# Kernel tuning notes

Hardware: AMD Instinct MI355X
Metric: run time of the kernel (lower is better)

The kernel has to match this reference:

```python
import jax, jax.numpy as jnp
import numpy as np

G = 8            # n_group
C = 256          # input_dim / channels
N_MEM = C // G   # 32
ALPHA = 0.4      # w_alpha
EPS = 1e-5
SLOPE = 0.01     # LeakyReLU negative slope


def _lrelu(x):
    return jnp.where(x >= 0, x, SLOPE * x)


def _mlp(x, ws, bs):
    # torch nn.Linear convention: y = x @ W.T + b; lrelu on all but last layer
    n = len(ws)
    for i in range(n):
        x = x @ ws[i].T + bs[i]
        if i < n - 1:
            x = _lrelu(x)
    return x


def _wct(c_A, s_B, mask, ct_ws, ct_bs, mu_ws, mu_bs):
    B, Cc, H, W = c_A.shape
    n_mem = Cc // G
    # style -> per-group coloring matrices  (Get.coloring, vectorized over groups)
    s_CT = _mlp(s_B.reshape(B * G, n_mem), ct_ws, ct_bs).reshape(B, G, n_mem, n_mem)
    D = jnp.sqrt(jnp.sum(s_CT ** 2, axis=2, keepdims=True))        # [B,G,1,n_mem]
    U = s_CT / D                                                    # column-normalized
    UDU = jnp.einsum('bgij,bgkj->bgik', s_CT, U)                    # [B,G,n_mem,n_mem]
    # torch.cat(U_arr, dim=0) is group-major: index g*B+b
    eigen_s = jnp.transpose(U, (1, 0, 2, 3)).reshape(G * B, n_mem, n_mem)
    X = jnp.tile(UDU.reshape(B, Cc, n_mem), (1, 1, G)) * mask       # [B,C,C]
    s_mu = _mlp(s_B, mu_ws, mu_bs)[:, :, None, None]                # [B,C,1,1]
    # per-group covariance of mean-centered content
    c_g = jnp.transpose(c_A, (1, 0, 2, 3)).reshape(G, n_mem, B * H * W)
    c_g = c_g - jnp.mean(c_g, axis=2, keepdims=True)
    cov_c = jnp.einsum('gin,gjn->gij', c_g, c_g) / (B * H * W - 1) \
        + EPS * jnp.eye(n_mem, dtype=c_A.dtype)
    # centered content, reinterpreted as [B, C, H*W] (matches torch view/permute)
    whitend = jnp.transpose(c_g.reshape(Cc, B, H * W), (1, 0, 2))
    colored = jnp.einsum('bcd,bdn->bcn', X, whitend).reshape(B, Cc, H, W)
    out = ALPHA * (colored + s_mu) + (1.0 - ALPHA) * c_A
    return out, cov_c, eigen_s


def setup_inputs():
    key = jax.random.key(0)
    ks = jax.random.split(key, 16)
    B, H, W = 4, 128, 128
    c_A = jax.random.normal(ks[0], (B, C, H, W), dtype=jnp.float32)
    s_B = jax.random.normal(ks[1], (B, C), dtype=jnp.float32)
    # block-diagonal group mask [1, C, C]
    m = np.zeros((C, C), dtype=np.float32)
    for g in range(G):
        m[g * N_MEM:(g + 1) * N_MEM, g * N_MEM:(g + 1) * N_MEM] = 1.0
    mask = jnp.asarray(m)[None]

    def lin(k, o, i):
        return jax.random.normal(k, (o, i), dtype=jnp.float32) * (1.0 / np.sqrt(i))

    inp = {'c_A': c_A, 's_B': s_B, 'mask': mask}
    dims_ct = [(256, 32), (256, 256), (256, 256), (256, 256), (1024, 256)]
    for j, (o, i) in enumerate(dims_ct):
        inp['ct_w%d' % j] = lin(ks[2 + j], o, i)
        inp['ct_b%d' % j] = jnp.zeros((o,), dtype=jnp.float32)
    dims_mu = [(256, 256), (256, 256), (256, 256)]
    for j, (o, i) in enumerate(dims_mu):
        inp['mu_w%d' % j] = lin(ks[8 + j], o, i)
        inp['mu_b%d' % j] = jnp.zeros((o,), dtype=jnp.float32)
    return inp


def reference(c_A, s_B, mask, ct_w0, ct_b0, ct_w1, ct_b1, ct_w2, ct_b2,
              ct_w3, ct_b3, ct_w4, ct_b4, mu_w0, mu_b0, mu_w1, mu_b1,
              mu_w2, mu_b2):
    ct_ws = (ct_w0, ct_w1, ct_w2, ct_w3, ct_w4)
    ct_bs = (ct_b0, ct_b1, ct_b2, ct_b3, ct_b4)
    mu_ws = (mu_w0, mu_w1, mu_w2)
    mu_bs = (mu_b0, mu_b1, mu_b2)
    return _wct(c_A, s_B, mask, ct_ws, ct_bs, mu_ws, mu_bs)
```

## Files before the change

### kernel.cpp

```cpp
#include <hip/hip_runtime.h>
#include <hip/hip_bf16.h>

typedef __bf16 bf16x8 __attribute__((ext_vector_type(8)));
typedef float  f32x16 __attribute__((ext_vector_type(16)));

#define ALPHA_W 0.4f
#define NTOT 65536.0f

#define OUT_MAIN 16777216
#define OUT_COV  (OUT_MAIN)
#define OUT_EIG  (OUT_MAIN + 8192)

#define WS_PSXY  0
#define WS_PSX   524288
#define WS_XA    540672
#define WS_XB    548864
#define WS_MUA   557056
#define WS_MUB   558080
#define WS_SMU   559104
#define WS_CT    560128

struct WP {
    const float* cw0; const float* cb0;
    const float* cw1; const float* cb1;
    const float* cw2; const float* cb2;
    const float* cw3; const float* cb3;
    const float* cw4; const float* cb4;
    const float* mw0; const float* mb0;
    const float* mw1; const float* mb1;
    const float* mw2; const float* mb2;
};

struct SJ { const float* X; const float* W; const float* B; float* Y; int ld; int act; };

__device__ __forceinline__ float lrelu(float x) { return x >= 0.f ? x : 0.01f * x; }

template<int ROWS, int IN, int KS, int NCB, int ACT>
__device__ __forceinline__ void lin_block(const float* __restrict__ X,
                                          const float* __restrict__ Wg,
                                          const float* __restrict__ Bs,
                                          float* __restrict__ Y, int ld,
                                          int bidl, int tid) {
    constexpr int SL = IN / KS;
    constexpr int SF4 = SL / 4;
    int s = tid % KS;
    int r = (tid / KS) % ROWS;
    int c = tid / (KS * ROWS);
    int col = bidl * NCB + c;
    const float4* wp = (const float4*)(Wg + (size_t)col * IN + s * SL);
    const float4* xp = (const float4*)(X + r * IN + s * SL);
    float a0 = 0.f, a1 = 0.f, a2 = 0.f, a3 = 0.f;
    #pragma unroll
    for (int i = 0; i < SF4; ++i) {
        float4 wv = wp[i];
        float4 xv = xp[i];
        a0 = fmaf(wv.x, xv.x, a0); a1 = fmaf(wv.y, xv.y, a1);
        a2 = fmaf(wv.z, xv.z, a2); a3 = fmaf(wv.w, xv.w, a3);
    }
    float v = (a0 + a1) + (a2 + a3);
    #pragma unroll
    for (int m = 1; m < KS; m <<= 1) v += __shfl_xor(v, m, 64);
    if (s == 0) {
        float o = v + Bs[col];
        if (ACT) o = lrelu(o);
        Y[(size_t)r * ld + col] = o;
    }
}

__global__ __launch_bounds__(256, 2) void front(const float* __restrict__ cA,
                                                const float* __restrict__ sB,
                                                WP wp,
                                                float* __restrict__ pSXY,
                                                float* __restrict__ pSX,
                                                float* __restrict__ XA,
                                                float* __restrict__ MUA) {
    int bid = blockIdx.x;
    int tid = threadIdx.x;
    if (bid < 64) {
        if (bid < 32) {
            lin_block<32, 32, 1, 8, 1>(sB, wp.cw0, wp.cb0, XA, 256, bid, tid);
        } else {
            lin_block<4, 256, 8, 8, 1>(sB, wp.mw0, wp.mb0, MUA, 256, bid - 32, tid);
        }
        return;
    }
    int gbid = bid - 64;
    int g = gbid >> 6, slice = gbid & 63;
    int w = tid >> 6, l = tid & 63;
    int col = l & 31, kq = l >> 5;
    int nbase = slice * 1024 + w * 256;
    int b = nbase >> 14, hw0 = nbase & 16383;
    const float* base = cA + (((size_t)(b * 256 + g * 32 + col)) << 14) + hw0 + kq * 8;
    f32x16 acc;
    #pragma unroll
    for (int r = 0; r < 16; r++) acc[r] = 0.f;
    float s0 = 0.f, s1 = 0.f;
    #pragma unroll 8
    for (int it = 0; it < 16; ++it) {
        float4 f0 = *(const float4*)(base + it * 16);
        float4 f1 = *(const float4*)(base + it * 16 + 4);
        s0 += (f0.x + f0.y) + (f0.z + f0.w);
        s1 += (f1.x + f1.y) + (f1.z + f1.w);
        bf16x8 v;
        v[0] = (__bf16)f0.x; v[1] = (__bf16)f0.y; v[2] = (__bf16)f0.z; v[3] = (__bf16)f0.w;
        v[4] = (__bf16)f1.x; v[5] = (__bf16)f1.y; v[6] = (__bf16)f1.z; v[7] = (__bf16)f1.w;
        acc = __builtin_amdgcn_mfma_f32_32x32x16_bf16(v, v, acc, 0, 0, 0);
    }
    __shared__ float red[4][1024];
    __shared__ float sxr[4][64];
    sxr[w][l] = s0 + s1;
    #pragma unroll
    for (int r = 0; r < 16; r++) {
        int i = (r & 3) + 8 * (r >> 2) + 4 * kq;
        red[w][i * 32 + col] = acc[r];
    }
    __syncthreads();
    for (int e = tid; e < 1024; e += 256)
        pSXY[(size_t)gbid * 1024 + e] = red[0][e] + red[1][e] + red[2][e] + red[3][e];
    if (tid < 32) {
        float v = 0.f;
        #pragma unroll
        for (int ww = 0; ww < 4; ww++) v += sxr[ww][tid] + sxr[ww][tid + 32];
        pSX[gbid * 32 + tid] = v;
    }
}

__global__ __launch_bounds__(256) void stage(SJ a, SJ m, int nbA) {
    int bid = blockIdx.x, tid = threadIdx.x;
    if (bid < nbA) {
        if (a.act) lin_block<32, 256, 4, 2, 1>(a.X, a.W, a.B, a.Y, a.ld, bid, tid);
        else       lin_block<32, 256, 4, 2, 0>(a.X, a.W, a.B, a.Y, a.ld, bid, tid);
    } else {
        int bl = bid - nbA;
        if (m.act) lin_block<4, 256, 8, 8, 1>(m.X, m.W, m.B, m.Y, m.ld, bl, tid);
        else       lin_block<4, 256, 8, 8, 0>(m.X, m.W, m.B, m.Y, m.ld, bl, tid);
    }
}

__global__ __launch_bounds__(256) void color_fused(const float* __restrict__ cA,
                                                   const float* __restrict__ CT,
                                                   const float* __restrict__ SMU,
                                                   const float* __restrict__ pSX,
                                                   const float* __restrict__ pSXY,
                                                   float* __restrict__ out) {
    __shared__ float sct[32 * 33];
    __shared__ float sctd[32 * 33];
    __shared__ float Ml[1024];
    __shared__ float tl[32];
    __shared__ float sxg[32];
    __shared__ float dinv[32];
    __shared__ float xs[2][2048];
    int bid = blockIdx.x;
    int tid = threadIdx.x;

    if (bid >= 1024) {
        int g = bid - 1024;
        if (tid < 32) {
            float s = 0.f;
            #pragma unroll
            for (int sl = 0; sl < 64; sl++) s += pSX[(g * 64 + sl) * 32 + tid];
            sxg[tid] = s * (1.0f / NTOT);
        }
        __syncthreads();
        float* cov = out + OUT_COV + (size_t)g * 1024;
        for (int e = tid; e < 1024; e += 256) {
            float s = 0.f;
            #pragma unroll
            for (int sl = 0; sl < 64; sl++) s += pSXY[(size_t)(g * 64 + sl) * 1024 + e];
            int i = e >> 5, jj = e & 31;
            float vv = (s - NTOT * sxg[i] * sxg[jj]) * (1.0f / (NTOT - 1.0f));
            if (i == jj) vv += 1e-5f;
            cov[e] = vv;
        }
        return;
    }

    int bg = bid >> 5, chunk = bid & 31;
    int b = bg >> 3, g = bg & 7;

    for (int e = tid; e < 1024; e += 256) sct[(e >> 5) * 33 + (e & 31)] = CT[(size_t)bg * 1024 + e];
    if (tid < 32) {
        float s = 0.f;
        #pragma unroll
        for (int sl = 0; sl < 64; sl++) s += pSX[(g * 64 + sl) * 32 + tid];
        sxg[tid] = s * (1.0f / NTOT);
    }
    __syncthreads();
    if (tid < 32) {
        float s = 0.f;
        #pragma unroll
        for (int i = 0; i < 32; i++) { float v = sct[i * 33 + tid]; s = fmaf(v, v, s); }
        dinv[tid] = 1.0f / sqrtf(s);
    }
    __syncthreads();
    for (int e = tid; e < 1024; e += 256) {
        int i = e >> 5, j = e & 31;
        sctd[i * 33 + j] = sct[i * 33 + j] * dinv[j];
    }
    __syncthreads();
    if (chunk == 0) {
        float* eig = out + OUT_EIG + (size_t)(g * 4 + b) * 1024;
        for (int e = tid; e < 1024; e += 256) eig[e] = sctd[(e >> 5) * 33 + (e & 31)];
    }
    for (int e = tid; e < 1024; e += 256) {
        int i = e >> 5, k = e & 31;
        float s = 0.f;
        #pragma unroll
        for (int j = 0; j < 32; j++) s = fmaf(sct[i * 33 + j], sctd[k * 33 + j], s);
        Ml[e] = ALPHA_W * s + (i == k ? (1.0f - ALPHA_W) : 0.0f);
    }
    __syncthreads();
    if (tid < 32) {
        float s = 0.f;
        #pragma unroll
        for (int k = 0; k < 32; k++) s = fmaf(Ml[tid * 32 + k], sxg[k], s);
        tl[tid] = ALPHA_W * SMU[bg * 32 + tid] - s + (1.0f - ALPHA_W) * sxg[tid];
    }

    int n = tid & 63, ih = tid >> 6;
    size_t cbase = (((size_t)(b * 256 + g * 32)) << 14) + chunk * 512;
    int srow = tid >> 3, scol = (tid & 7) * 8;
    size_t obase = (((size_t)(b * 256 + g * 32 + ih * 8)) << 14) + chunk * 512 + n;
    const float* src0 = cA + cbase + (size_t)srow * 16384 + scol;
    float4 u0 = *(const float4*)src0;
    float4 u1 = *(const float4*)(src0 + 4);
    for (int tile = 0; tile < 8; ++tile) {
        float* xd = &xs[tile & 1][srow * 64 + scol];
        *(float4*)xd = u0;
        *(float4*)(xd + 4) = u1;
        if (tile < 7) {
            const float* src = cA + cbase + (size_t)srow * 16384 + (tile + 1) * 64 + scol;
            u0 = *(const float4*)src;
            u1 = *(const float4*)(src + 4);
        }
        __syncthreads();
        const float* xb = xs[tile & 1];
        float acc[8];
        #pragma unroll
        for (int i = 0; i < 8; i++) acc[i] = tl[ih * 8 + i];
        #pragma unroll
        for (int k = 0; k < 32; k++) {
            float xv = xb[k * 64 + n];
            #pragma unroll
            for (int i = 0; i < 8; i++) acc[i] = fmaf(Ml[(ih * 8 + i) * 32 + k], xv, acc[i]);
        }
        float* dst = out + obase + tile * 64;
        #pragma unroll
        for (int i = 0; i < 8; i++) dst[(size_t)i << 14] = acc[i];
    }
}

extern "C" void kernel_launch(void* const* d_in, const int* in_sizes, int n_in,
                              void* d_out, int out_size, void* d_ws, size_t ws_size,
                              hipStream_t stream) {
    (void)in_sizes; (void)n_in; (void)out_size; (void)ws_size;
    const float* cA = (const float*)d_in[0];
    const float* sB = (const float*)d_in[1];
    WP wp;
    wp.cw0 = (const float*)d_in[3];  wp.cb0 = (const float*)d_in[4];
    wp.cw1 = (const float*)d_in[5];  wp.cb1 = (const float*)d_in[6];
    wp.cw2 = (const float*)d_in[7];  wp.cb2 = (const float*)d_in[8];
    wp.cw3 = (const float*)d_in[9];  wp.cb3 = (const float*)d_in[10];
    wp.cw4 = (const float*)d_in[11]; wp.cb4 = (const float*)d_in[12];
    wp.mw0 = (const float*)d_in[13]; wp.mb0 = (const float*)d_in[14];
    wp.mw1 = (const float*)d_in[15]; wp.mb1 = (const float*)d_in[16];
    wp.mw2 = (const float*)d_in[17]; wp.mb2 = (const float*)d_in[18];
    float* W = (float*)d_ws;
    float* out = (float*)d_out;

    front<<<576, 256, 0, stream>>>(cA, sB, wp, W + WS_PSXY, W + WS_PSX,
                                   W + WS_XA, W + WS_MUA);
    SJ a, m;
    a = {W + WS_XA, wp.cw1, wp.cb1, W + WS_XB, 256, 1};
    m = {W + WS_MUA, wp.mw1, wp.mb1, W + WS_MUB, 256, 1};
    stage<<<160, 256, 0, stream>>>(a, m, 128);
    a = {W + WS_XB, wp.cw2, wp.cb2, W + WS_XA, 256, 1};
    m = {W + WS_MUB, wp.mw2, wp.mb2, W + WS_SMU, 256, 0};
    stage<<<160, 256, 0, stream>>>(a, m, 128);
    a = {W + WS_XA, wp.cw3, wp.cb3, W + WS_XB, 256, 1};
    stage<<<128, 256, 0, stream>>>(a, a, 128);
    a = {W + WS_XB, wp.cw4, wp.cb4, W + WS_CT, 1024, 0};
    stage<<<512, 256, 0, stream>>>(a, a, 512);

    color_fused<<<1032, 256, 0, stream>>>(cA, W + WS_CT, W + WS_SMU,
                                          W + WS_PSX, W + WS_PSXY, out);
}
```

Measured before the change: 197.3 us.

## Fuse MLP stages into front kernel with grid barriers and precompute coloring matrix

New measurement: 253.9 us. 28.7% more time.

```diff
diff --git a/kernel.cpp b/kernel.cpp
--- a/kernel.cpp
+++ b/kernel.cpp
@@ -19,6 +19,8 @@
 #define WS_MUB   558080
 #define WS_SMU   559104
 #define WS_CT    560128
+#define WS_M     592896
+#define WS_BAR   625664
 
 struct WP {
     const float* cw0; const float* cb0;
@@ -31,9 +33,19 @@
     const float* mw2; const float* mb2;
 };
 
-struct SJ { const float* X; const float* W; const float* B; float* Y; int ld; int act; };
-
 __device__ __forceinline__ float lrelu(float x) { return x >= 0.f ? x : 0.01f * x; }
+
+__device__ __forceinline__ void mlp_bar(int* bar, int phase, int nb, int tid) {
+    __syncthreads();
+    if (tid == 0) {
+        __threadfence();
+        __hip_atomic_fetch_add(&bar[phase], 1, __ATOMIC_RELEASE, __HIP_MEMORY_SCOPE_AGENT);
+        while (__hip_atomic_load(&bar[phase], __ATOMIC_ACQUIRE, __HIP_MEMORY_SCOPE_AGENT) < nb)
+            __builtin_amdgcn_s_sleep(2);
+        __threadfence();
+    }
+    __syncthreads();
+}
 
 template<int ROWS, int IN, int KS, int NCB, int ACT>
 __device__ __forceinline__ void lin_block(const float* __restrict__ X,
@@ -67,89 +79,132 @@
     }
 }
 
+__global__ void zero_bar(int* bar) {
+    if (threadIdx.x < 16) bar[threadIdx.x] = 0;
+}
+
 __global__ __launch_bounds__(256, 2) void front(const float* __restrict__ cA,
                                                 const float* __restrict__ sB,
                                                 WP wp,
-                                                float* __restrict__ pSXY,
-                                                float* __restrict__ pSX,
-                                                float* __restrict__ XA,
-                                                float* __restrict__ MUA) {
+                                                float* __restrict__ Wf,
+                                                float* __restrict__ out) {
+    __shared__ float smem[4352];
     int bid = blockIdx.x;
     int tid = threadIdx.x;
+
     if (bid < 64) {
+        float* XA  = Wf + WS_XA;
+        float* XB  = Wf + WS_XB;
+        float* MUA = Wf + WS_MUA;
+        float* MUB = Wf + WS_MUB;
+        float* SMU = Wf + WS_SMU;
+        float* CT  = Wf + WS_CT;
+        int* bar = (int*)(Wf + WS_BAR);
+        if (bid < 32) lin_block<32, 32, 1, 8, 1>(sB, wp.cw0, wp.cb0, XA, 256, bid, tid);
+        else          lin_block<4, 256, 8, 8, 1>(sB, wp.mw0, wp.mb0, MUA, 256, bid - 32, tid);
+        mlp_bar(bar, 0, 64, tid);
+        lin_block<32, 256, 2, 4, 1>(XA, wp.cw1, wp.cb1, XB, 256, bid, tid);
+        lin_block<4, 256, 16, 4, 1>(MUA, wp.mw1, wp.mb1, MUB, 256, bid, tid);
+        mlp_bar(bar, 1, 64, tid);
+        lin_block<32, 256, 2, 4, 1>(XB, wp.cw2, wp.cb2, XA, 256, bid, tid);
+        lin_block<4, 256, 16, 4, 0>(MUB, wp.mw2, wp.mb2, SMU, 256, bid, tid);
+        mlp_bar(bar, 2, 64, tid);
+        lin_block<32, 256, 2, 4, 1>(XA, wp.cw3, wp.cb3, XB, 256, bid, tid);
+        mlp_bar(bar, 3, 64, tid);
+        lin_block<32, 256, 2, 4, 0>(XB, wp.cw4,          wp.cb4,       CT,       1024, bid, tid);
+        lin_block<32, 256, 2, 4, 0>(XB, wp.cw4 + 65536,  wp.cb4 + 256, CT + 256, 1024, bid, tid);
+        lin_block<32, 256, 2, 4, 0>(XB, wp.cw4 + 131072, wp.cb4 + 512, CT + 512, 1024, bid, tid);
+        lin_block<32, 256, 2, 4, 0>(XB, wp.cw4 + 196608, wp.cb4 + 768, CT + 768, 1024, bid, tid);
+        mlp_bar(bar, 4, 64, tid);
         if (bid < 32) {
-            lin_block<32, 32, 1, 8, 1>(sB, wp.cw0, wp.cb0, XA, 256, bid, tid);
-        } else {
-            lin_block<4, 256, 8, 8, 1>(sB, wp.mw0, wp.mb0, MUA, 256, bid - 32, tid);
-        }
-        return;
-    }
-    int gbid = bid - 64;
-    int g = gbid >> 6, slice = gbid & 63;
-    int w = tid >> 6, l = tid & 63;
-    int col = l & 31, kq = l >> 5;
-    int nbase = slice * 1024 + w * 256;
-    int b = nbase >> 14, hw0 = nbase & 16383;
-    const float* base = cA + (((size_t)(b * 256 + g * 32 + col)) << 14) + hw0 + kq * 8;
-    f32x16 acc;
-    #pragma unroll
-    for (int r = 0; r < 16; r++) acc[r] = 0.f;
-    float s0 = 0.f, s1 = 0.f;
-    #pragma unroll 8
-    for (int it = 0; it < 16; ++it) {
-        float4 f0 = *(const float4*)(base + it * 16);
-        float4 f1 = *(const float4*)(base + it * 16 + 4);
-        s0 += (f0.x + f0.y) + (f0.z + f0.w);
-        s1 += (f1.x + f1.y) + (f1.z + f1.w);
-        bf16x8 v;
-        v[0] = (__bf16)f0.x; v[1] = (__bf16)f0.y; v[2] = (__bf16)f0.z; v[3] = (__bf16)f0.w;
-        v[4] = (__bf16)f1.x; v[5] = (__bf16)f1.y; v[6] = (__bf16)f1.z; v[7] = (__bf16)f1.w;
-        acc = __builtin_amdgcn_mfma_f32_32x32x16_bf16(v, v, acc, 0, 0, 0);
-    }
-    __shared__ float red[4][1024];
-    __shared__ float sxr[4][64];
-    sxr[w][l] = s0 + s1;
-    #pragma unroll
-    for (int r = 0; r < 16; r++) {
-        int i = (r & 3) + 8 * (r >> 2) + 4 * kq;
-        red[w][i * 32 + col] = acc[r];
-    }
-    __syncthreads();
-    for (int e = tid; e < 1024; e += 256)
-        pSXY[(size_t)gbid * 1024 + e] = red[0][e] + red[1][e] + red[2][e] + red[3][e];
-    if (tid < 32) {
-        float v = 0.f;
-        #pragma unroll
-        for (int ww = 0; ww < 4; ww++) v += sxr[ww][tid] + sxr[ww][tid + 32];
-        pSX[gbid * 32 + tid] = v;
-    }
-}
-
-__global__ __launch_bounds__(256) void stage(SJ a, SJ m, int nbA) {
-    int bid = blockIdx.x, tid = threadIdx.x;
-    if (bid < nbA) {
-        if (a.act) lin_block<32, 256, 4, 2, 1>(a.X, a.W, a.B, a.Y, a.ld, bid, tid);
-        else       lin_block<32, 256, 4, 2, 0>(a.X, a.W, a.B, a.Y, a.ld, bid, tid);
-    } else {
-        int bl = bid - nbA;
-        if (m.act) lin_block<4, 256, 8, 8, 1>(m.X, m.W, m.B, m.Y, m.ld, bl, tid);
-        else       lin_block<4, 256, 8, 8, 0>(m.X, m.W, m.B, m.Y, m.ld, bl, tid);
+            float* sct  = smem;
+            float* uu   = smem + 1056;
+            float* dinv = smem + 2112;
+            int b = bid >> 3, g = bid & 7;
+            for (int e = tid; e < 1024; e += 256)
+                sct[(e >> 5) * 33 + (e & 31)] = CT[(size_t)bid * 1024 + e];
+            __syncthreads();
+            if (tid < 32) {
+                float s = 0.f;
+                #pragma unroll
+                for (int i = 0; i < 32; i++) { float v = sct[i * 33 + tid]; s = fmaf(v, v, s); }
+                dinv[tid] = 1.0f / sqrtf(s);
+            }
+            __syncthreads();
+            float* eig = out + OUT_EIG + (size_t)(g * 4 + b) * 1024;
+            for (int e = tid; e < 1024; e += 256) {
+                int i = e >> 5, j = e & 31;
+                float u = sct[i * 33 + j] * dinv[j];
+                uu[i * 33 + j] = u;
+                eig[e] = u;
+            }
+            __syncthreads();
+            float* Mo = Wf + WS_M + (size_t)bid * 1024;
+            for (int e = tid; e < 1024; e += 256) {
+                int i = e >> 5, k = e & 31;
+                float s = 0.f;
+                #pragma unroll
+                for (int j = 0; j < 32; j++) s = fmaf(sct[i * 33 + j], uu[k * 33 + j], s);
+                Mo[e] = ALPHA_W * s + (i == k ? (1.0f - ALPHA_W) : 0.0f);
+            }
+            __syncthreads();
+        }
+    }
+
+    float* pSXY = Wf + WS_PSXY;
+    float* pSX  = Wf + WS_PSX;
+    int gbid = bid;
+    {
+        int g = gbid >> 6, slice = gbid & 63;
+        int w = tid >> 6, l = tid & 63;
+        int col = l & 31, kq = l >> 5;
+        int nbase = slice * 1024 + w * 256;
+        int b = nbase >> 14, hw0 = nbase & 16383;
+        const float* base = cA + (((size_t)(b * 256 + g * 32 + col)) << 14) + hw0 + kq * 8;
+        f32x16 acc;
+        #pragma unroll
+        for (int r = 0; r < 16; r++) acc[r] = 0.f;
+        float s0 = 0.f, s1 = 0.f;
+        #pragma unroll 8
+        for (int it = 0; it < 16; ++it) {
+            float4 f0 = *(const float4*)(base + it * 16);
+            float4 f1 = *(const float4*)(base + it * 16 + 4);
+            s0 += (f0.x + f0.y) + (f0.z + f0.w);
+            s1 += (f1.x + f1.y) + (f1.z + f1.w);
+            bf16x8 v;
+            v[0] = (__bf16)f0.x; v[1] = (__bf16)f0.y; v[2] = (__bf16)f0.z; v[3] = (__bf16)f0.w;
+            v[4] = (__bf16)f1.x; v[5] = (__bf16)f1.y; v[6] = (__bf16)f1.z; v[7] = (__bf16)f1.w;
+            acc = __builtin_amdgcn_mfma_f32_32x32x16_bf16(v, v, acc, 0, 0, 0);
+        }
+        float* red = smem;
+        float* sxr = smem + 4096;
+        sxr[w * 64 + l] = s0 + s1;
+        #pragma unroll
+        for (int r = 0; r < 16; r++) {
+            int i = (r & 3) + 8 * (r >> 2) + 4 * kq;
+            red[w * 1024 + i * 32 + col] = acc[r];
+        }
+        __syncthreads();
+        for (int e = tid; e < 1024; e += 256)
+            pSXY[(size_t)gbid * 1024 + e] = red[e] + red[1024 + e] + red[2048 + e] + red[3072 + e];
+        if (tid < 32) {
+            float v = 0.f;
+            #pragma unroll
+            for (int ww = 0; ww < 4; ww++) v += sxr[ww * 64 + tid] + sxr[ww * 64 + tid + 32];
+            pSX[gbid * 32 + tid] = v;
+        }
     }
 }
 
 __global__ __launch_bounds__(256) void color_fused(const float* __restrict__ cA,
-                                                   const float* __restrict__ CT,
+                                                   const float* __restrict__ M,
                                                    const float* __restrict__ SMU,
                                                    const float* __restrict__ pSX,
                                                    const float* __restrict__ pSXY,
                                                    float* __restrict__ out) {
-    __shared__ float sct[32 * 33];
-    __shared__ float sctd[32 * 33];
     __shared__ float Ml[1024];
     __shared__ float tl[32];
     __shared__ float sxg[32];
-    __shared__ float dinv[32];
-    __shared__ float xs[2][2048];
     int bid = blockIdx.x;
     int tid = threadIdx.x;
 
@@ -178,7 +233,7 @@
     int bg = bid >> 5, chunk = bid & 31;
     int b = bg >> 3, g = bg & 7;
 
-    for (int e = tid; e < 1024; e += 256) sct[(e >> 5) * 33 + (e & 31)] = CT[(size_t)bg * 1024 + e];
+    for (int e = tid; e < 1024; e += 256) Ml[e] = M[(size_t)bg * 1024 + e];
     if (tid < 32) {
         float s = 0.f;
         #pragma unroll
@@ -189,64 +244,52 @@
     if (tid < 32) {
         float s = 0.f;
         #pragma unroll
-        for (int i = 0; i < 32; i++) { float v = sct[i * 33 + tid]; s = fmaf(v, v, s); }
-        dinv[tid] = 1.0f / sqrtf(s);
-    }
-    __syncthreads();
-    for (int e = tid; e < 1024; e += 256) {
-        int i = e >> 5, j = e & 31;
-        sctd[i * 33 + j] = sct[i * 33 + j] * dinv[j];
-    }
-    __syncthreads();
-    if (chunk == 0) {
-        float* eig = out + OUT_EIG + (size_t)(g * 4 + b) * 1024;
-        for (int e = tid; e < 1024; e += 256) eig[e] = sctd[(e >> 5) * 33 + (e & 31)];
-    }
-    for (int e = tid; e < 1024; e += 256) {
-        int i = e >> 5, k = e & 31;
-        float s = 0.f;
-        #pragma unroll
-        for (int j = 0; j < 32; j++) s = fmaf(sct[i * 33 + j], sctd[k * 33 + j], s);
-        Ml[e] = ALPHA_W * s + (i == k ? (1.0f - ALPHA_W) : 0.0f);
-    }
-    __syncthreads();
-    if (tid < 32) {
-        float s = 0.f;
-        #pragma unroll
         for (int k = 0; k < 32; k++) s = fmaf(Ml[tid * 32 + k], sxg[k], s);
         tl[tid] = ALPHA_W * SMU[bg * 32 + tid] - s + (1.0f - ALPHA_W) * sxg[tid];
     }
-
-    int n = tid & 63, ih = tid >> 6;
-    size_t cbase = (((size_t)(b * 256 + g * 32)) << 14) + chunk * 512;
-    int srow = tid >> 3, scol = (tid & 7) * 8;
-    size_t obase = (((size_t)(b * 256 + g * 32 + ih * 8)) << 14) + chunk * 512 + n;
-    const float* src0 = cA + cbase + (size_t)srow * 16384 + scol;
-    float4 u0 = *(const float4*)src0;
-    float4 u1 = *(const float4*)(src0 + 4);
-    for (int tile = 0; tile < 8; ++tile) {
-        float* xd = &xs[tile & 1][srow * 64 + scol];
-        *(float4*)xd = u0;
-        *(float4*)(xd + 4) = u1;
-        if (tile < 7) {
-            const float* src = cA + cbase + (size_t)srow * 16384 + (tile + 1) * 64 + scol;
-            u0 = *(const float4*)src;
-            u1 = *(const float4*)(src + 4);
-        }
-        __syncthreads();
-        const float* xb = xs[tile & 1];
-        float acc[8];
-        #pragma unroll
-        for (int i = 0; i < 8; i++) acc[i] = tl[ih * 8 + i];
-        #pragma unroll
-        for (int k = 0; k < 32; k++) {
-            float xv = xb[k * 64 + n];
-            #pragma unroll
-            for (int i = 0; i < 8; i++) acc[i] = fmaf(Ml[(ih * 8 + i) * 32 + k], xv, acc[i]);
-        }
-        float* dst = out + obase + tile * 64;
-        #pragma unroll
-        for (int i = 0; i < 8; i++) dst[(size_t)i << 14] = acc[i];
+    __syncthreads();
+
+    int ci = tid >> 6;
+    int pj = tid & 63;
+    size_t rowbase = ((size_t)(b * 256 + g * 32)) << 14;
+    int px = chunk * 512 + pj * 8;
+    const float* xsrc = cA + rowbase + px;
+    float* dst = out + rowbase + (((size_t)ci * 8) << 14) + px;
+
+    float acc[8][8];
+    #pragma unroll
+    for (int c = 0; c < 8; ++c) {
+        float t0 = tl[ci * 8 + c];
+        #pragma unroll
+        for (int j = 0; j < 8; ++j) acc[c][j] = t0;
+    }
+    #pragma unroll 4
+    for (int k = 0; k < 32; ++k) {
+        const float* xk = xsrc + ((size_t)k << 14);
+        float4 x0 = *(const float4*)xk;
+        float4 x1 = *(const float4*)(xk + 4);
+        float xv0 = x0.x, xv1 = x0.y, xv2 = x0.z, xv3 = x0.w;
+        float xv4 = x1.x, xv5 = x1.y, xv6 = x1.z, xv7 = x1.w;
+        #pragma unroll
+        for (int c = 0; c < 8; ++c) {
+            float m = Ml[(ci * 8 + c) * 32 + k];
+            acc[c][0] = fmaf(m, xv0, acc[c][0]);
+            acc[c][1] = fmaf(m, xv1, acc[c][1]);
+            acc[c][2] = fmaf(m, xv2, acc[c][2]);
+            acc[c][3] = fmaf(m, xv3, acc[c][3]);
+            acc[c][4] = fmaf(m, xv4, acc[c][4]);
+            acc[c][5] = fmaf(m, xv5, acc[c][5]);
+            acc[c][6] = fmaf(m, xv6, acc[c][6]);
+            acc[c][7] = fmaf(m, xv7, acc[c][7]);
+        }
+    }
+    #pragma unroll
+    for (int c = 0; c < 8; ++c) {
+        float4 o0 = {acc[c][0], acc[c][1], acc[c][2], acc[c][3]};
+        float4 o1 = {acc[c][4], acc[c][5], acc[c][6], acc[c][7]};
+        float* d = dst + (((size_t)c) << 14);
+        *(float4*)d = o0;
+        *(float4*)(d + 4) = o1;
     }
 }
 
@@ -268,20 +311,8 @@
     float* W = (float*)d_ws;
     float* out = (float*)d_out;
 
-    front<<<576, 256, 0, stream>>>(cA, sB, wp, W + WS_PSXY, W + WS_PSX,
-                                   W + WS_XA, W + WS_MUA);
-    SJ a, m;
-    a = {W + WS_XA, wp.cw1, wp.cb1, W + WS_XB, 256, 1};
-    m = {W + WS_MUA, wp.mw1, wp.mb1, W + WS_MUB, 256, 1};
-    stage<<<160, 256, 0, stream>>>(a, m, 128);
-    a = {W + WS_XB, wp.cw2, wp.cb2, W + WS_XA, 256, 1};
-    m = {W + WS_MUB, wp.mw2, wp.mb2, W + WS_SMU, 256, 0};
-    stage<<<160, 256, 0, stream>>>(a, m, 128);
-    a = {W + WS_XA, wp.cw3, wp.cb3, W + WS_XB, 256, 1};
-    stage<<<128, 256, 0, stream>>>(a, a, 128);
-    a = {W + WS_XB, wp.cw4, wp.cb4, W + WS_CT, 1024, 0};
-    stage<<<512, 256, 0, stream>>>(a, a, 512);
-
-    color_fused<<<1032, 256, 0, stream>>>(cA, W + WS_CT, W + WS_SMU,
+    zero_bar<<<1, 64, 0, stream>>>((int*)(W + WS_BAR));
+    front<<<512, 256, 0, stream>>>(cA, sB, wp, W, out);
+    color_fused<<<1032, 256, 0, stream>>>(cA, W + WS_M, W + WS_SMU,
                                           W + WS_PSX, W + WS_PSXY, out);
 }
```

## Split coloring into finalize and register-tiled color kernel; parametrize covariance slicing

Applied to the files above, without the earlier changes.

Result: slower. 232.4 us (+17.8%).

```diff
diff --git a/kernel.cpp b/kernel.cpp
--- a/kernel.cpp
+++ b/kernel.cpp
@@ -10,15 +10,6 @@
 #define OUT_MAIN 16777216
 #define OUT_COV  (OUT_MAIN)
 #define OUT_EIG  (OUT_MAIN + 8192)
-
-#define WS_PSXY  0
-#define WS_PSX   524288
-#define WS_XA    540672
-#define WS_XB    548864
-#define WS_MUA   557056
-#define WS_MUB   558080
-#define WS_SMU   559104
-#define WS_CT    560128
 
 struct WP {
     const float* cw0; const float* cb0;
@@ -67,6 +58,7 @@
     }
 }
 
+template<int SPG>
 __global__ __launch_bounds__(256, 2) void front(const float* __restrict__ cA,
                                                 const float* __restrict__ sB,
                                                 WP wp,
@@ -84,11 +76,13 @@
         }
         return;
     }
+    constexpr int PSZ = 65536 / SPG;
+    constexpr int ITS = PSZ / 64;
     int gbid = bid - 64;
-    int g = gbid >> 6, slice = gbid & 63;
+    int g = gbid / SPG, slice = gbid % SPG;
     int w = tid >> 6, l = tid & 63;
     int col = l & 31, kq = l >> 5;
-    int nbase = slice * 1024 + w * 256;
+    int nbase = slice * PSZ + w * (PSZ / 4);
     int b = nbase >> 14, hw0 = nbase & 16383;
     const float* base = cA + (((size_t)(b * 256 + g * 32 + col)) << 14) + hw0 + kq * 8;
     f32x16 acc;
@@ -96,7 +90,7 @@
     for (int r = 0; r < 16; r++) acc[r] = 0.f;
     float s0 = 0.f, s1 = 0.f;
     #pragma unroll 8
-    for (int it = 0; it < 16; ++it) {
+    for (int it = 0; it < ITS; ++it) {
         float4 f0 = *(const float4*)(base + it * 16);
         float4 f1 = *(const float4*)(base + it * 16 + 4);
         s0 += (f0.x + f0.y) + (f0.z + f0.w);
@@ -137,123 +131,141 @@
     }
 }
 
-__global__ __launch_bounds__(256) void color_fused(const float* __restrict__ cA,
-                                                   const float* __restrict__ CT,
+template<int SPG>
+__global__ __launch_bounds__(256, 2) void finalize(const float* __restrict__ CT,
                                                    const float* __restrict__ SMU,
+                                                   const float* __restrict__ pSXY,
                                                    const float* __restrict__ pSX,
-                                                   const float* __restrict__ pSXY,
+                                                   float* __restrict__ M,
+                                                   float* __restrict__ T,
                                                    float* __restrict__ out) {
-    __shared__ float sct[32 * 33];
-    __shared__ float sctd[32 * 33];
-    __shared__ float Ml[1024];
-    __shared__ float tl[32];
+    int bid = blockIdx.x, t = threadIdx.x;
     __shared__ float sxg[32];
-    __shared__ float dinv[32];
-    __shared__ float xs[2][2048];
-    int bid = blockIdx.x;
-    int tid = threadIdx.x;
-
-    if (bid >= 1024) {
-        int g = bid - 1024;
-        if (tid < 32) {
+    if (bid < 32) {
+        int b = bid >> 3, g = bid & 7;
+        __shared__ float sct[32 * 33], uu[32 * 33], ud[32 * 33], dinv[32];
+        for (int e = t; e < 1024; e += 256) sct[(e >> 5) * 33 + (e & 31)] = CT[bid * 1024 + e];
+        if (t < 32) {
+            float s = 0.f;
+            #pragma unroll 8
+            for (int sl = 0; sl < SPG; sl++) s += pSX[(g * SPG + sl) * 32 + t];
+            sxg[t] = s * (1.0f / NTOT);
+        }
+        __syncthreads();
+        if (t < 32) {
             float s = 0.f;
             #pragma unroll
-            for (int sl = 0; sl < 64; sl++) s += pSX[(g * 64 + sl) * 32 + tid];
-            sxg[tid] = s * (1.0f / NTOT);
+            for (int i = 0; i < 32; i++) { float v = sct[i * 33 + t]; s = fmaf(v, v, s); }
+            dinv[t] = 1.0f / sqrtf(s);
+        }
+        __syncthreads();
+        float* eig = out + OUT_EIG + (size_t)(g * 4 + b) * 1024;
+        for (int e = t; e < 1024; e += 256) {
+            int i = e >> 5, jj = e & 31;
+            float u = sct[i * 33 + jj] * dinv[jj];
+            uu[i * 33 + jj] = u;
+            eig[e] = u;
+        }
+        __syncthreads();
+        float* Mo = M + (size_t)bid * 1024;
+        for (int e = t; e < 1024; e += 256) {
+            int i = e >> 5, k = e & 31;
+            float s = 0.f;
+            #pragma unroll
+            for (int jv = 0; jv < 32; jv++) s = fmaf(sct[i * 33 + jv], uu[k * 33 + jv], s);
+            ud[i * 33 + k] = s;
+            Mo[e] = ALPHA_W * s + (i == k ? (1.0f - ALPHA_W) : 0.0f);
+        }
+        __syncthreads();
+        if (t < 32) {
+            float s = 0.f;
+            #pragma unroll
+            for (int k = 0; k < 32; k++) s = fmaf(ud[t * 33 + k], sxg[k], s);
+            T[bid * 32 + t] = ALPHA_W * (SMU[bid * 32 + t] - s);
+        }
+    } else {
+        int g = bid - 32;
+        if (t < 32) {
+            float s = 0.f;
+            #pragma unroll 8
+            for (int sl = 0; sl < SPG; sl++) s += pSX[(g * SPG + sl) * 32 + t];
+            sxg[t] = s * (1.0f / NTOT);
         }
         __syncthreads();
         float* cov = out + OUT_COV + (size_t)g * 1024;
-        for (int e = tid; e < 1024; e += 256) {
-            float s = 0.f;
-            #pragma unroll
-            for (int sl = 0; sl < 64; sl++) s += pSXY[(size_t)(g * 64 + sl) * 1024 + e];
+        for (int e = t; e < 1024; e += 256) {
+            float s = 0.f;
+            #pragma unroll 8
+            for (int sl = 0; sl < SPG; sl++) s += pSXY[(size_t)(g * SPG + sl) * 1024 + e];
             int i = e >> 5, jj = e & 31;
             float vv = (s - NTOT * sxg[i] * sxg[jj]) * (1.0f / (NTOT - 1.0f));
             if (i == jj) vv += 1e-5f;
             cov[e] = vv;
         }
-        return;
-    }
-
+    }
+}
+
+__global__ __launch_bounds__(256) void color_k(const float* __restrict__ cA,
+                                               const float* __restrict__ M,
+                                               const float* __restrict__ T,
+                                               float* __restrict__ out) {
+    __shared__ float Ml[1024];
+    __shared__ float tl[32];
+    int bid = blockIdx.x;
+    int tid = threadIdx.x;
     int bg = bid >> 5, chunk = bid & 31;
     int b = bg >> 3, g = bg & 7;
 
-    for (int e = tid; e < 1024; e += 256) sct[(e >> 5) * 33 + (e & 31)] = CT[(size_t)bg * 1024 + e];
-    if (tid < 32) {
-        float s = 0.f;
+    for (int e = tid; e < 1024; e += 256) Ml[e] = M[(size_t)bg * 1024 + e];
+    if (tid < 32) tl[tid] = T[bg * 32 + tid];
+    __syncthreads();
+
+    int ci = tid >> 6;
+    int pj = tid & 63;
+    size_t rowbase = ((size_t)(b * 256 + g * 32)) << 14;
+    int px = chunk * 512 + pj * 8;
+    const float* xsrc = cA + rowbase + px;
+    float* dst = out + rowbase + (((size_t)ci * 8) << 14) + px;
+
+    float acc[8][8];
+    #pragma unroll
+    for (int c = 0; c < 8; ++c) {
+        float t0 = tl[ci * 8 + c];
         #pragma unroll
-        for (int sl = 0; sl < 64; sl++) s += pSX[(g * 64 + sl) * 32 + tid];
-        sxg[tid] = s * (1.0f / NTOT);
-    }
-    __syncthreads();
-    if (tid < 32) {
-        float s = 0.f;
+        for (int j = 0; j < 8; ++j) acc[c][j] = t0;
+    }
+    #pragma unroll 4
+    for (int k = 0; k < 32; ++k) {
+        const float* xk = xsrc + ((size_t)k << 14);
+        float4 x0 = *(const float4*)xk;
+        float4 x1 = *(const float4*)(xk + 4);
         #pragma unroll
-        for (int i = 0; i < 32; i++) { float v = sct[i * 33 + tid]; s = fmaf(v, v, s); }
-        dinv[tid] = 1.0f / sqrtf(s);
-    }
-    __syncthreads();
-    for (int e = tid; e < 1024; e += 256) {
-        int i = e >> 5, j = e & 31;
-        sctd[i * 33 + j] = sct[i * 33 + j] * dinv[j];
-    }
-    __syncthreads();
-    if (chunk == 0) {
-        float* eig = out + OUT_EIG + (size_t)(g * 4 + b) * 1024;
-        for (int e = tid; e < 1024; e += 256) eig[e] = sctd[(e >> 5) * 33 + (e & 31)];
-    }
-    for (int e = tid; e < 1024; e += 256) {
-        int i = e >> 5, k = e & 31;
-        float s = 0.f;
-        #pragma unroll
-        for (int j = 0; j < 32; j++) s = fmaf(sct[i * 33 + j], sctd[k * 33 + j], s);
-        Ml[e] = ALPHA_W * s + (i == k ? (1.0f - ALPHA_W) : 0.0f);
-    }
-    __syncthreads();
-    if (tid < 32) {
-        float s = 0.f;
-        #pragma unroll
-        for (int k = 0; k < 32; k++) s = fmaf(Ml[tid * 32 + k], sxg[k], s);
-        tl[tid] = ALPHA_W * SMU[bg * 32 + tid] - s + (1.0f - ALPHA_W) * sxg[tid];
-    }
-
-    int n = tid & 63, ih = tid >> 6;
-    size_t cbase = (((size_t)(b * 256 + g * 32)) << 14) + chunk * 512;
-    int srow = tid >> 3, scol = (tid & 7) * 8;
-    size_t obase = (((size_t)(b * 256 + g * 32 + ih * 8)) << 14) + chunk * 512 + n;
-    const float* src0 = cA + cbase + (size_t)srow * 16384 + scol;
-    float4 u0 = *(const float4*)src0;
-    float4 u1 = *(const float4*)(src0 + 4);
-    for (int tile = 0; tile < 8; ++tile) {
-        float* xd = &xs[tile & 1][srow * 64 + scol];
-        *(float4*)xd = u0;
-        *(float4*)(xd + 4) = u1;
-        if (tile < 7) {
-            const float* src = cA + cbase + (size_t)srow * 16384 + (tile + 1) * 64 + scol;
-            u0 = *(const float4*)src;
-            u1 = *(const float4*)(src + 4);
-        }
-        __syncthreads();
-        const float* xb = xs[tile & 1];
-        float acc[8];
-        #pragma unroll
-        for (int i = 0; i < 8; i++) acc[i] = tl[ih * 8 + i];
-        #pragma unroll
-        for (int k = 0; k < 32; k++) {
-            float xv = xb[k * 64 + n];
-            #pragma unroll
-            for (int i = 0; i < 8; i++) acc[i] = fmaf(Ml[(ih * 8 + i) * 32 + k], xv, acc[i]);
-        }
-        float* dst = out + obase + tile * 64;
-        #pragma unroll
-        for (int i = 0; i < 8; i++) dst[(size_t)i << 14] = acc[i];
+        for (int c = 0; c < 8; ++c) {
+            float m = Ml[(ci * 8 + c) * 32 + k];
+            acc[c][0] = fmaf(m, x0.x, acc[c][0]);
+            acc[c][1] = fmaf(m, x0.y, acc[c][1]);
+            acc[c][2] = fmaf(m, x0.z, acc[c][2]);
+            acc[c][3] = fmaf(m, x0.w, acc[c][3]);
+            acc[c][4] = fmaf(m, x1.x, acc[c][4]);
+            acc[c][5] = fmaf(m, x1.y, acc[c][5]);
+            acc[c][6] = fmaf(m, x1.z, acc[c][6]);
+            acc[c][7] = fmaf(m, x1.w, acc[c][7]);
+        }
+    }
+    #pragma unroll
+    for (int c = 0; c < 8; ++c) {
+        float4 o0 = {acc[c][0], acc[c][1], acc[c][2], acc[c][3]};
+        float4 o1 = {acc[c][4], acc[c][5], acc[c][6], acc[c][7]};
+        float* d = dst + (((size_t)c) << 14);
+        *(float4*)d = o0;
+        *(float4*)(d + 4) = o1;
     }
 }
 
 extern "C" void kernel_launch(void* const* d_in, const int* in_sizes, int n_in,
                               void* d_out, int out_size, void* d_ws, size_t ws_size,
                               hipStream_t stream) {
-    (void)in_sizes; (void)n_in; (void)out_size; (void)ws_size;
+    (void)in_sizes; (void)n_in; (void)out_size;
     const float* cA = (const float*)d_in[0];
     const float* sB = (const float*)d_in[1];
     WP wp;
@@ -268,20 +280,38 @@
     float* W = (float*)d_ws;
     float* out = (float*)d_out;
 
-    front<<<576, 256, 0, stream>>>(cA, sB, wp, W + WS_PSXY, W + WS_PSX,
-                                   W + WS_XA, W + WS_MUA);
+    bool big = ws_size >= (size_t)6 * 1024 * 1024;
+    int NSL = big ? 1024 : 512;
+    size_t oPSX = (size_t)NSL * 1024;
+    size_t base = oPSX + (size_t)NSL * 32;
+    float* pSXY = W;
+    float* pSX  = W + oPSX;
+    float* XA   = W + base;
+    float* XB   = XA + 8192;
+    float* MUA  = XB + 8192;
+    float* MUB  = MUA + 1024;
+    float* SMU  = MUB + 1024;
+    float* CT   = SMU + 1024;
+    float* Mw   = CT + 32768;
+    float* Tw   = Mw + 32768;
+
+    if (big) front<128><<<64 + 1024, 256, 0, stream>>>(cA, sB, wp, pSXY, pSX, XA, MUA);
+    else     front<64><<<64 + 512, 256, 0, stream>>>(cA, sB, wp, pSXY, pSX, XA, MUA);
+
     SJ a, m;
-    a = {W + WS_XA, wp.cw1, wp.cb1, W + WS_XB, 256, 1};
-    m = {W + WS_MUA, wp.mw1, wp.mb1, W + WS_MUB, 256, 1};
+    a = {XA, wp.cw1, wp.cb1, XB, 256, 1};
+    m = {MUA, wp.mw1, wp.mb1, MUB, 256, 1};
     stage<<<160, 256, 0, stream>>>(a, m, 128);
-    a = {W + WS_XB, wp.cw2, wp.cb2, W + WS_XA, 256, 1};
-    m = {W + WS_MUB, wp.mw2, wp.mb2, W + WS_SMU, 256, 0};
+    a = {XB, wp.cw2, wp.cb2, XA, 256, 1};
+    m = {MUB, wp.mw2, wp.mb2, SMU, 256, 0};
     stage<<<160, 256, 0, stream>>>(a, m, 128);
-    a = {W + WS_XA, wp.cw3, wp.cb3, W + WS_XB, 256, 1};
+    a = {XA, wp.cw3, wp.cb3, XB, 256, 1};
     stage<<<128, 256, 0, stream>>>(a, a, 128);
-    a = {W + WS_XB, wp.cw4, wp.cb4, W + WS_CT, 1024, 0};
+    a = {XB, wp.cw4, wp.cb4, CT, 1024, 0};
     stage<<<512, 256, 0, stream>>>(a, a, 512);
 
-    color_fused<<<1032, 256, 0, stream>>>(cA, W + WS_CT, W + WS_SMU,
-                                          W + WS_PSX, W + WS_PSXY, out);
-}
+    if (big) finalize<128><<<40, 256, 0, stream>>>(CT, SMU, pSXY, pSX, Mw, Tw, out);
+    else     finalize<64><<<40, 256, 0, stream>>>(CT, SMU, pSXY, pSX, Mw, Tw, out);
+
+    color_k<<<1024, 256, 0, stream>>>(cA, Mw, Tw, out);
+}
```
